# Performance work log

Measured on AMD Instinct MI355X. Metric: run time of the kernel, lower is better.

Reference implementation:

```python
import jax, jax.numpy as jnp
import numpy as np

B, S, D, T, H = 4, 2048, 1024, 5, 8


def setup_inputs() -> dict:
    key = jax.random.key(0)
    ks = jax.random.split(key, 12)
    sc = 0.02  # small init scale for weights so attention logits stay sane
    return {
        "x": jax.random.normal(ks[0], (B, S, D), jnp.float32),
        "time_steps": jax.random.randint(ks[1], (B, S), 0, T),
        "gamma": jnp.ones((T, D), jnp.float32),
        "beta": jax.random.normal(ks[2], (T, D), jnp.float32) * sc,
        "decay": jnp.ones((T,), jnp.float32),
        "shift_W": jax.random.normal(ks[3], (D, D), jnp.float32) * sc,
        "shift_b": jax.random.normal(ks[4], (D,), jnp.float32) * sc,
        "in_proj_W": jax.random.normal(ks[5], (3 * D, D), jnp.float32) * sc,
        "in_proj_b": jax.random.normal(ks[6], (3 * D,), jnp.float32) * sc,
        "out_proj_W": jax.random.normal(ks[7], (D, D), jnp.float32) * sc,
        "out_proj_b": jax.random.normal(ks[8], (D,), jnp.float32) * sc,
    }


def reference(x, time_steps, gamma, beta, decay, shift_W, shift_b,
              in_proj_W, in_proj_b, out_proj_W, out_proj_b):
    eps = 1e-5
    T_ = gamma.shape[0]
    b_, s_, d_ = x.shape
    hd = d_ // H

    # --- per-token indexed LayerNorm + decay (vectorized gather of norm params) ---
    idx = jnp.clip(time_steps, 0, T_ - 1)              # safe gather index [B,S]
    mu = jnp.mean(x, axis=-1, keepdims=True)
    var = jnp.mean(jnp.square(x - mu), axis=-1, keepdims=True)
    xn = (x - mu) * jax.lax.rsqrt(var + eps)           # [B,S,D]
    normed = (xn * gamma[idx] + beta[idx]) * decay[idx][..., None]
    x = jnp.where((time_steps < T_)[..., None], normed, x)

    # --- residual temporal shift (Linear) ---
    x = x + x @ shift_W.T + shift_b

    # --- torch-style MultiheadAttention(x, x, x), batch_first ---
    qkv = x @ in_proj_W.T + in_proj_b                  # [B,S,3D]
    q, k, v = jnp.split(qkv, 3, axis=-1)
    q = q.reshape(b_, s_, H, hd)
    k = k.reshape(b_, s_, H, hd)
    v = v.reshape(b_, s_, H, hd)
    scale = 1.0 / jnp.sqrt(jnp.asarray(hd, x.dtype))
    scores = jnp.einsum('bqhd,bkhd->bhqk', q, k) * scale   # [B,H,S,S]
    attn = jax.nn.softmax(scores, axis=-1)
    ctx = jnp.einsum('bhqk,bkhd->bqhd', attn, v).reshape(b_, s_, d_)
    attended = ctx @ out_proj_W.T + out_proj_b
    return x + attended
```

## Files before the change

kernel.cpp:

```cpp
#include <hip/hip_runtime.h>
#include <math.h>

#define B_ 4
#define S_ 2048
#define D_ 1024
#define T_ 5
#define H_ 8
#define HD_ 128
#define M_ (B_*S_)

typedef __bf16 bf16x8 __attribute__((ext_vector_type(8)));
typedef float  f32x4  __attribute__((ext_vector_type(4)));

__device__ __forceinline__ float bf2f(unsigned short u) {
    union { unsigned int i; float f; } c; c.i = ((unsigned int)u) << 16; return c.f;
}
__device__ __forceinline__ unsigned short f2bf(float f) {
    union { float f; unsigned int i; } c; c.f = f;
    unsigned int u = c.i;
    u += 0x7fffu + ((u >> 16) & 1u);
    return (unsigned short)(u >> 16);
}

__device__ __forceinline__ void gll16(const void* g, void* l) {
    __builtin_amdgcn_global_load_lds(
        (const __attribute__((address_space(1))) void*)g,
        (__attribute__((address_space(3))) void*)l, 16, 0, 0);
}

__global__ __launch_bounds__(256) void f2bf_kernel(
    const float* __restrict__ src, unsigned short* __restrict__ dst)
{
    int i = (blockIdx.x * 256 + threadIdx.x) * 4;
    float4 v = *(const float4*)(src + i);
    ushort4 o;
    o.x = f2bf(v.x); o.y = f2bf(v.y); o.z = f2bf(v.z); o.w = f2bf(v.w);
    *(ushort4*)(dst + i) = o;
}

__global__ __launch_bounds__(256) void ln_kernel(
    const float* __restrict__ x, const int* __restrict__ ts,
    const float* __restrict__ gamma, const float* __restrict__ beta,
    const float* __restrict__ decay, unsigned short* __restrict__ out)
{
    int row = blockIdx.x;
    int tid = threadIdx.x;
    float4 v = ((const float4*)(x + (size_t)row * D_))[tid];
    float s  = v.x + v.y + v.z + v.w;
    float s2 = v.x*v.x + v.y*v.y + v.z*v.z + v.w*v.w;
    #pragma unroll
    for (int off = 32; off; off >>= 1) {
        s  += __shfl_down(s,  off);
        s2 += __shfl_down(s2, off);
    }
    __shared__ float ps[4], ps2[4];
    if ((tid & 63) == 0) { ps[tid >> 6] = s; ps2[tid >> 6] = s2; }
    __syncthreads();
    float tot  = ps[0]  + ps[1]  + ps[2]  + ps[3];
    float tot2 = ps2[0] + ps2[1] + ps2[2] + ps2[3];
    float mu   = tot  * (1.0f / D_);
    float var  = tot2 * (1.0f / D_) - mu * mu;
    float rstd = rsqrtf(var + 1e-5f);

    int t  = ts[row];
    int tc = min(max(t, 0), T_ - 1);
    float4 g = ((const float4*)(gamma + (size_t)tc * D_))[tid];
    float4 b = ((const float4*)(beta  + (size_t)tc * D_))[tid];
    float dec = decay[tc];

    float4 o;
    o.x = ((v.x - mu) * rstd * g.x + b.x) * dec;
    o.y = ((v.y - mu) * rstd * g.y + b.y) * dec;
    o.z = ((v.z - mu) * rstd * g.z + b.z) * dec;
    o.w = ((v.w - mu) * rstd * g.w + b.w) * dec;
    if (t >= T_) o = v;
    ushort4 ob;
    ob.x = f2bf(o.x); ob.y = f2bf(o.y); ob.z = f2bf(o.z); ob.w = f2bf(o.w);
    ((ushort4*)(out + (size_t)row * D_))[tid] = ob;
}

__global__ __launch_bounds__(256) void gemm_mfma(
    const unsigned short* __restrict__ A,
    const unsigned short* __restrict__ Wt,
    const float* __restrict__ bias,
    const float* __restrict__ ResF,
    const unsigned short* __restrict__ ResB,
    float* __restrict__ Cf,
    unsigned short* __restrict__ Cb,
    int M, int N, int K)
{
    __shared__ __align__(16) unsigned short As[128 * 32];
    __shared__ __align__(16) unsigned short Bs[128 * 32];
    int tid  = threadIdx.x;
    int w    = tid >> 6, lane = tid & 63;
    int lm   = lane & 15, quad = lane >> 4;
    int wm   = w & 1,  wn   = w >> 1;
    int i0 = blockIdx.y * 128, j0 = blockIdx.x * 128;

    f32x4 acc[4][4];
    #pragma unroll
    for (int mt = 0; mt < 4; ++mt)
        #pragma unroll
        for (int nt = 0; nt < 4; ++nt)
            acc[mt][nt] = (f32x4){0.f, 0.f, 0.f, 0.f};

    int c0 = w * 128 + lane;
    int r0 = c0 >> 2,   k80 = (c0 & 3) * 8;
    int c1 = c0 + 64;
    int r1 = c1 >> 2,   k81 = (c1 & 3) * 8;

    for (int kt = 0; kt < K; kt += 32) {
        __syncthreads();
        gll16(A  + (size_t)(i0 + r0) * K + kt + k80, As + (size_t)(w * 128 + 0 ) * 8);
        gll16(A  + (size_t)(i0 + r1) * K + kt + k81, As + (size_t)(w * 128 + 64) * 8);
        gll16(Wt + (size_t)(j0 + r0) * K + kt + k80, Bs + (size_t)(w * 128 + 0 ) * 8);
        gll16(Wt + (size_t)(j0 + r1) * K + kt + k81, Bs + (size_t)(w * 128 + 64) * 8);
        __syncthreads();

        bf16x8 af[4], bfr[4];
        #pragma unroll
        for (int mt = 0; mt < 4; ++mt)
            af[mt] = *(const bf16x8*)&As[(wm * 64 + mt * 16 + lm) * 32 + quad * 8];
        #pragma unroll
        for (int nt = 0; nt < 4; ++nt)
            bfr[nt] = *(const bf16x8*)&Bs[(wn * 64 + nt * 16 + lm) * 32 + quad * 8];
        #pragma unroll
        for (int mt = 0; mt < 4; ++mt)
            #pragma unroll
            for (int nt = 0; nt < 4; ++nt)
                acc[mt][nt] = __builtin_amdgcn_mfma_f32_16x16x32_bf16(
                    af[mt], bfr[nt], acc[mt][nt], 0, 0, 0);
    }

    #pragma unroll
    for (int nt = 0; nt < 4; ++nt) {
        int j = j0 + wn * 64 + nt * 16 + lm;
        float bj = bias[j];
        #pragma unroll
        for (int mt = 0; mt < 4; ++mt) {
            #pragma unroll
            for (int r = 0; r < 4; ++r) {
                int i = i0 + wm * 64 + mt * 16 + quad * 4 + r;
                size_t off = (size_t)i * N + j;
                float v = acc[mt][nt][r] + bj;
                if (ResF) v += ResF[off];
                else if (ResB) v += bf2f(ResB[off]);
                if (Cf) Cf[off] = v;
                if (Cb) Cb[off] = f2bf(v);
            }
        }
    }
}

__global__ __launch_bounds__(256) void transpose_v(
    const unsigned short* __restrict__ qkv, unsigned short* __restrict__ vt)
{
    __shared__ unsigned short Ts[64][72];
    int t = threadIdx.x;
    int s0 = blockIdx.x * 64, c0 = blockIdx.y * 64, b = blockIdx.z;
    int r  = t >> 2, cg = (t & 3) * 16;
    const unsigned short* src =
        qkv + (size_t)(b * S_ + s0 + r) * (3 * D_) + 2 * D_ + c0 + cg;
    *(bf16x8*)&Ts[r][cg]     = *(const bf16x8*)(src);
    *(bf16x8*)&Ts[r][cg + 8] = *(const bf16x8*)(src + 8);
    __syncthreads();
    int dd = t >> 2, sg = (t & 3) * 16;
    unsigned short tmp[16];
    #pragma unroll
    for (int j = 0; j < 16; ++j) tmp[j] = Ts[sg + j][dd];
    unsigned short* dst = vt + ((size_t)b * D_ + c0 + dd) * S_ + s0 + sg;
    *(bf16x8*)dst       = *(bf16x8*)&tmp[0];
    *(bf16x8*)(dst + 8) = *(bf16x8*)&tmp[8];
}

__global__ __launch_bounds__(256, 2) void flash_mfma(
    const unsigned short* __restrict__ qkv,
    const unsigned short* __restrict__ vt,
    unsigned short* __restrict__ ctx)
{
    __shared__ unsigned short Ks [64][136];
    __shared__ unsigned short Vts[128][72];
    __shared__ unsigned short Ps [4][32][72];

    int tid  = threadIdx.x;
    int w    = tid >> 6, lane = tid & 63;
    int lm   = lane & 15, quad = lane >> 4;
    int qt = blockIdx.x, h = blockIdx.y, b = blockIdx.z;
    const int rs = 3 * D_;
    const float scale = 0.08838834764831844f;
    size_t qbase  = (size_t)b * S_ * rs + (size_t)h * HD_;
    size_t kbase  = qbase + D_;
    size_t vtbase = ((size_t)b * H_ + h) * (size_t)HD_ * S_;
    int q0 = qt * 128 + w * 32;

    bf16x8 qf[2][4];
    #pragma unroll
    for (int mt = 0; mt < 2; ++mt)
        #pragma unroll
        for (int kc = 0; kc < 4; ++kc) {
            bf16x8 raw = *(const bf16x8*)(
                qkv + qbase + (size_t)(q0 + mt * 16 + lm) * rs + kc * 32 + quad * 8);
            bf16x8 sc;
            #pragma unroll
            for (int j = 0; j < 8; ++j) {
                unsigned short u;
                __builtin_memcpy(&u, (const char*)&raw + 2 * j, 2);
                u = f2bf(bf2f(u) * scale);
                __builtin_memcpy((char*)&sc + 2 * j, &u, 2);
            }
            qf[mt][kc] = sc;
        }

    f32x4 oacc[2][8];
    #pragma unroll
    for (int mt = 0; mt < 2; ++mt)
        #pragma unroll
        for (int n = 0; n < 8; ++n)
            oacc[mt][n] = (f32x4){0.f, 0.f, 0.f, 0.f};
    float lst[2][4];
    #pragma unroll
    for (int mt = 0; mt < 2; ++mt)
        #pragma unroll
        for (int r = 0; r < 4; ++r) lst[mt][r] = 0.f;

    for (int kt = 0; kt < S_ / 64; ++kt) {
        int k0 = kt * 64;
        __syncthreads();
        #pragma unroll
        for (int i = 0; i < 4; ++i) {
            int chunk = tid + 256 * i;
            int r = chunk >> 4, cc = chunk & 15;
            bf16x8 kv8 = *(const bf16x8*)(
                qkv + kbase + (size_t)(k0 + r) * rs + cc * 8);
            *(bf16x8*)&Ks[r][cc * 8] = kv8;
        }
        #pragma unroll
        for (int i = 0; i < 4; ++i) {
            int chunk = tid + 256 * i;
            int d = chunk >> 3, cc = chunk & 7;
            bf16x8 vv8 = *(const bf16x8*)(
                vt + vtbase + (size_t)d * S_ + k0 + cc * 8);
            *(bf16x8*)&Vts[d][cc * 8] = vv8;
        }
        __syncthreads();

        f32x4 sacc[2][4];
        #pragma unroll
        for (int mt = 0; mt < 2; ++mt)
            #pragma unroll
            for (int n = 0; n < 4; ++n)
                sacc[mt][n] = (f32x4){0.f, 0.f, 0.f, 0.f};
        #pragma unroll
        for (int n = 0; n < 4; ++n) {
            bf16x8 bk[4];
            #pragma unroll
            for (int kc = 0; kc < 4; ++kc)
                bk[kc] = *(const bf16x8*)&Ks[n * 16 + lm][kc * 32 + quad * 8];
            #pragma unroll
            for (int mt = 0; mt < 2; ++mt)
                #pragma unroll
                for (int kc = 0; kc < 4; ++kc)
                    sacc[mt][n] = __builtin_amdgcn_mfma_f32_16x16x32_bf16(
                        qf[mt][kc], bk[kc], sacc[mt][n], 0, 0, 0);
        }

        #pragma unroll
        for (int mt = 0; mt < 2; ++mt) {
            #pragma unroll
            for (int r = 0; r < 4; ++r) {
                float p0 = __expf(sacc[mt][0][r]);
                float p1 = __expf(sacc[mt][1][r]);
                float p2 = __expf(sacc[mt][2][r]);
                float p3 = __expf(sacc[mt][3][r]);
                lst[mt][r] += (p0 + p1) + (p2 + p3);
                int row = mt * 16 + quad * 4 + r;
                Ps[w][row][ 0 + lm] = f2bf(p0);
                Ps[w][row][16 + lm] = f2bf(p1);
                Ps[w][row][32 + lm] = f2bf(p2);
                Ps[w][row][48 + lm] = f2bf(p3);
            }
        }

        bf16x8 pa[2][2];
        #pragma unroll
        for (int mt = 0; mt < 2; ++mt)
            #pragma unroll
            for (int kc = 0; kc < 2; ++kc)
                pa[mt][kc] = *(const bf16x8*)&Ps[w][mt * 16 + lm][kc * 32 + quad * 8];
        #pragma unroll
        for (int n = 0; n < 8; ++n) {
            bf16x8 bv0 = *(const bf16x8*)&Vts[n * 16 + lm][quad * 8];
            bf16x8 bv1 = *(const bf16x8*)&Vts[n * 16 + lm][32 + quad * 8];
            #pragma unroll
            for (int mt = 0; mt < 2; ++mt) {
                oacc[mt][n] = __builtin_amdgcn_mfma_f32_16x16x32_bf16(
                    pa[mt][0], bv0, oacc[mt][n], 0, 0, 0);
                oacc[mt][n] = __builtin_amdgcn_mfma_f32_16x16x32_bf16(
                    pa[mt][1], bv1, oacc[mt][n], 0, 0, 0);
            }
        }
    }

    float linv[2][4];
    #pragma unroll
    for (int mt = 0; mt < 2; ++mt)
        #pragma unroll
        for (int r = 0; r < 4; ++r) {
            float l = lst[mt][r];
            l += __shfl_xor(l, 1);
            l += __shfl_xor(l, 2);
            l += __shfl_xor(l, 4);
            l += __shfl_xor(l, 8);
            linv[mt][r] = 1.0f / l;
        }
    size_t rowbase = (size_t)b * S_ + (size_t)qt * 128 + w * 32;
    #pragma unroll
    for (int mt = 0; mt < 2; ++mt)
        #pragma unroll
        for (int r = 0; r < 4; ++r) {
            size_t row = rowbase + mt * 16 + quad * 4 + r;
            unsigned short* dst = ctx + row * D_ + h * HD_ + lm;
            #pragma unroll
            for (int n = 0; n < 8; ++n)
                dst[n * 16] = f2bf(oacc[mt][n][r] * linv[mt][r]);
        }
}

extern "C" void kernel_launch(void* const* d_in, const int* in_sizes, int n_in,
                              void* d_out, int out_size, void* d_ws, size_t ws_size,
                              hipStream_t stream) {
    (void)in_sizes; (void)n_in; (void)out_size; (void)ws_size;
    const float* x          = (const float*)d_in[0];
    const int*   ts         = (const int*)  d_in[1];
    const float* gamma      = (const float*)d_in[2];
    const float* beta       = (const float*)d_in[3];
    const float* decay      = (const float*)d_in[4];
    const float* shift_W    = (const float*)d_in[5];
    const float* shift_b    = (const float*)d_in[6];
    const float* in_proj_W  = (const float*)d_in[7];
    const float* in_proj_b  = (const float*)d_in[8];
    const float* out_proj_W = (const float*)d_in[9];
    const float* out_proj_b = (const float*)d_in[10];
    float* out = (float*)d_out;

    unsigned short* p     = (unsigned short*)d_ws;
    unsigned short* xln_b = p;
    unsigned short* qkv_b = xln_b + (size_t)M_ * D_;
    unsigned short* xs_b  = qkv_b + (size_t)M_ * 3 * D_;
    unsigned short* wsh_b = xs_b  + (size_t)M_ * D_;
    unsigned short* wip_b = wsh_b + (size_t)D_ * D_;
    unsigned short* wop_b = wip_b + (size_t)3 * D_ * D_;
    unsigned short* vt_b  = xs_b;
    unsigned short* ctx_b = xln_b;
    float* xs = out;

    f2bf_kernel<<<D_ * D_ / 1024,     256, 0, stream>>>(shift_W,    wsh_b);
    f2bf_kernel<<<3 * D_ * D_ / 1024, 256, 0, stream>>>(in_proj_W,  wip_b);
    f2bf_kernel<<<D_ * D_ / 1024,     256, 0, stream>>>(out_proj_W, wop_b);

    ln_kernel<<<M_, 256, 0, stream>>>(x, ts, gamma, beta, decay, xln_b);

    gemm_mfma<<<dim3(D_ / 128, M_ / 128), 256, 0, stream>>>(
        xln_b, wsh_b, shift_b, nullptr, xln_b, xs, xs_b, M_, D_, D_);
    gemm_mfma<<<dim3(3 * D_ / 128, M_ / 128), 256, 0, stream>>>(
        xs_b, wip_b, in_proj_b, nullptr, nullptr, nullptr, qkv_b, M_, 3 * D_, D_);

    transpose_v<<<dim3(S_ / 64, D_ / 64, B_), 256, 0, stream>>>(qkv_b, vt_b);
    flash_mfma<<<dim3(S_ / 128, H_, B_), 256, 0, stream>>>(qkv_b, vt_b, ctx_b);

    gemm_mfma<<<dim3(D_ / 128, M_ / 128), 256, 0, stream>>>(
        ctx_b, wop_b, out_proj_b, xs, nullptr, out, nullptr, M_, D_, D_);
}
```

Baseline: 407.3 us.

## Halve flash attention query tile per block and reorder grid for K/V reuse

The flash attention kernel now processes 64 query rows per block (16 per wave) instead of 128, which halves per-thread accumulator and Q-fragment registers and raises the launch-bounds occupancy target from 2 to 3 blocks per CU. The grid becomes 1D with the 32 (batch, head) pairs varying fastest, so concurrently running blocks span many heads, and there are twice as many blocks, which helps fill the GPU. The cost is that each block loads the same K/V tile into LDS for half as much MFMA work, doubling total K/V traffic and the number of block-wide syncs per unit of compute.

```diff
diff --git a/kernel.cpp b/kernel.cpp
--- a/kernel.cpp
+++ b/kernel.cpp
@@ -173,55 +173,50 @@
     *(bf16x8*)(dst + 8) = *(bf16x8*)&tmp[8];
 }
 
-__global__ __launch_bounds__(256, 2) void flash_mfma(
+__global__ __launch_bounds__(256, 3) void flash_mfma(
     const unsigned short* __restrict__ qkv,
     const unsigned short* __restrict__ vt,
     unsigned short* __restrict__ ctx)
 {
     __shared__ unsigned short Ks [64][136];
     __shared__ unsigned short Vts[128][72];
-    __shared__ unsigned short Ps [4][32][72];
+    __shared__ unsigned short Ps [4][16][72];
 
     int tid  = threadIdx.x;
     int w    = tid >> 6, lane = tid & 63;
     int lm   = lane & 15, quad = lane >> 4;
-    int qt = blockIdx.x, h = blockIdx.y, b = blockIdx.z;
+    int blk = blockIdx.x;
+    int bh  = blk & 31;
+    int qt  = blk >> 5;
+    int b   = bh >> 3, h = bh & 7;
     const int rs = 3 * D_;
     const float scale = 0.08838834764831844f;
     size_t qbase  = (size_t)b * S_ * rs + (size_t)h * HD_;
     size_t kbase  = qbase + D_;
     size_t vtbase = ((size_t)b * H_ + h) * (size_t)HD_ * S_;
-    int q0 = qt * 128 + w * 32;
-
-    bf16x8 qf[2][4];
-    #pragma unroll
-    for (int mt = 0; mt < 2; ++mt)
-        #pragma unroll
-        for (int kc = 0; kc < 4; ++kc) {
-            bf16x8 raw = *(const bf16x8*)(
-                qkv + qbase + (size_t)(q0 + mt * 16 + lm) * rs + kc * 32 + quad * 8);
-            bf16x8 sc;
-            #pragma unroll
-            for (int j = 0; j < 8; ++j) {
-                unsigned short u;
-                __builtin_memcpy(&u, (const char*)&raw + 2 * j, 2);
-                u = f2bf(bf2f(u) * scale);
-                __builtin_memcpy((char*)&sc + 2 * j, &u, 2);
-            }
-            qf[mt][kc] = sc;
-        }
-
-    f32x4 oacc[2][8];
-    #pragma unroll
-    for (int mt = 0; mt < 2; ++mt)
-        #pragma unroll
-        for (int n = 0; n < 8; ++n)
-            oacc[mt][n] = (f32x4){0.f, 0.f, 0.f, 0.f};
-    float lst[2][4];
-    #pragma unroll
-    for (int mt = 0; mt < 2; ++mt)
-        #pragma unroll
-        for (int r = 0; r < 4; ++r) lst[mt][r] = 0.f;
+    int q0 = qt * 64 + w * 16;
+
+    bf16x8 qf[4];
+    #pragma unroll
+    for (int kc = 0; kc < 4; ++kc) {
+        bf16x8 raw = *(const bf16x8*)(
+            qkv + qbase + (size_t)(q0 + lm) * rs + kc * 32 + quad * 8);
+        bf16x8 sc;
+        #pragma unroll
+        for (int j = 0; j < 8; ++j) {
+            unsigned short u;
+            __builtin_memcpy(&u, (const char*)&raw + 2 * j, 2);
+            u = f2bf(bf2f(u) * scale);
+            __builtin_memcpy((char*)&sc + 2 * j, &u, 2);
+        }
+        qf[kc] = sc;
+    }
+
+    f32x4 oacc[8];
+    #pragma unroll
+    for (int n = 0; n < 8; ++n)
+        oacc[n] = (f32x4){0.f, 0.f, 0.f, 0.f};
+    float lst[4] = {0.f, 0.f, 0.f, 0.f};
 
     for (int kt = 0; kt < S_ / 64; ++kt) {
         int k0 = kt * 64;
@@ -244,86 +239,68 @@
         }
         __syncthreads();
 
-        f32x4 sacc[2][4];
-        #pragma unroll
-        for (int mt = 0; mt < 2; ++mt)
+        f32x4 sacc[4];
+        #pragma unroll
+        for (int n = 0; n < 4; ++n)
+            sacc[n] = (f32x4){0.f, 0.f, 0.f, 0.f};
+        #pragma unroll
+        for (int n = 0; n < 4; ++n) {
             #pragma unroll
-            for (int n = 0; n < 4; ++n)
-                sacc[mt][n] = (f32x4){0.f, 0.f, 0.f, 0.f};
-        #pragma unroll
-        for (int n = 0; n < 4; ++n) {
-            bf16x8 bk[4];
-            #pragma unroll
-            for (int kc = 0; kc < 4; ++kc)
-                bk[kc] = *(const bf16x8*)&Ks[n * 16 + lm][kc * 32 + quad * 8];
-            #pragma unroll
-            for (int mt = 0; mt < 2; ++mt)
-                #pragma unroll
-                for (int kc = 0; kc < 4; ++kc)
-                    sacc[mt][n] = __builtin_amdgcn_mfma_f32_16x16x32_bf16(
-                        qf[mt][kc], bk[kc], sacc[mt][n], 0, 0, 0);
-        }
-
-        #pragma unroll
-        for (int mt = 0; mt < 2; ++mt) {
-            #pragma unroll
-            for (int r = 0; r < 4; ++r) {
-                float p0 = __expf(sacc[mt][0][r]);
-                float p1 = __expf(sacc[mt][1][r]);
-                float p2 = __expf(sacc[mt][2][r]);
-                float p3 = __expf(sacc[mt][3][r]);
-                lst[mt][r] += (p0 + p1) + (p2 + p3);
-                int row = mt * 16 + quad * 4 + r;
-                Ps[w][row][ 0 + lm] = f2bf(p0);
-                Ps[w][row][16 + lm] = f2bf(p1);
-                Ps[w][row][32 + lm] = f2bf(p2);
-                Ps[w][row][48 + lm] = f2bf(p3);
+            for (int kc = 0; kc < 4; ++kc) {
+                bf16x8 bk = *(const bf16x8*)&Ks[n * 16 + lm][kc * 32 + quad * 8];
+                sacc[n] = __builtin_amdgcn_mfma_f32_16x16x32_bf16(
+                    qf[kc], bk, sacc[n], 0, 0, 0);
             }
         }
 
-        bf16x8 pa[2][2];
-        #pragma unroll
-        for (int mt = 0; mt < 2; ++mt)
-            #pragma unroll
-            for (int kc = 0; kc < 2; ++kc)
-                pa[mt][kc] = *(const bf16x8*)&Ps[w][mt * 16 + lm][kc * 32 + quad * 8];
+        #pragma unroll
+        for (int r = 0; r < 4; ++r) {
+            float p0 = __expf(sacc[0][r]);
+            float p1 = __expf(sacc[1][r]);
+            float p2 = __expf(sacc[2][r]);
+            float p3 = __expf(sacc[3][r]);
+            lst[r] += (p0 + p1) + (p2 + p3);
+            int row = quad * 4 + r;
+            Ps[w][row][ 0 + lm] = f2bf(p0);
+            Ps[w][row][16 + lm] = f2bf(p1);
+            Ps[w][row][32 + lm] = f2bf(p2);
+            Ps[w][row][48 + lm] = f2bf(p3);
+        }
+
+        bf16x8 pa[2];
+        #pragma unroll
+        for (int kc = 0; kc < 2; ++kc)
+            pa[kc] = *(const bf16x8*)&Ps[w][lm][kc * 32 + quad * 8];
         #pragma unroll
         for (int n = 0; n < 8; ++n) {
             bf16x8 bv0 = *(const bf16x8*)&Vts[n * 16 + lm][quad * 8];
             bf16x8 bv1 = *(const bf16x8*)&Vts[n * 16 + lm][32 + quad * 8];
-            #pragma unroll
-            for (int mt = 0; mt < 2; ++mt) {
-                oacc[mt][n] = __builtin_amdgcn_mfma_f32_16x16x32_bf16(
-                    pa[mt][0], bv0, oacc[mt][n], 0, 0, 0);
-                oacc[mt][n] = __builtin_amdgcn_mfma_f32_16x16x32_bf16(
-                    pa[mt][1], bv1, oacc[mt][n], 0, 0, 0);
-            }
-        }
-    }
-
-    float linv[2][4];
-    #pragma unroll
-    for (int mt = 0; mt < 2; ++mt)
-        #pragma unroll
-        for (int r = 0; r < 4; ++r) {
-            float l = lst[mt][r];
-            l += __shfl_xor(l, 1);
-            l += __shfl_xor(l, 2);
-            l += __shfl_xor(l, 4);
-            l += __shfl_xor(l, 8);
-            linv[mt][r] = 1.0f / l;
-        }
-    size_t rowbase = (size_t)b * S_ + (size_t)qt * 128 + w * 32;
-    #pragma unroll
-    for (int mt = 0; mt < 2; ++mt)
-        #pragma unroll
-        for (int r = 0; r < 4; ++r) {
-            size_t row = rowbase + mt * 16 + quad * 4 + r;
-            unsigned short* dst = ctx + row * D_ + h * HD_ + lm;
-            #pragma unroll
-            for (int n = 0; n < 8; ++n)
-                dst[n * 16] = f2bf(oacc[mt][n][r] * linv[mt][r]);
-        }
+            oacc[n] = __builtin_amdgcn_mfma_f32_16x16x32_bf16(
+                pa[0], bv0, oacc[n], 0, 0, 0);
+            oacc[n] = __builtin_amdgcn_mfma_f32_16x16x32_bf16(
+                pa[1], bv1, oacc[n], 0, 0, 0);
+        }
+    }
+
+    float linv[4];
+    #pragma unroll
+    for (int r = 0; r < 4; ++r) {
+        float l = lst[r];
+        l += __shfl_xor(l, 1);
+        l += __shfl_xor(l, 2);
+        l += __shfl_xor(l, 4);
+        l += __shfl_xor(l, 8);
+        linv[r] = 1.0f / l;
+    }
+    size_t rowbase = (size_t)b * S_ + (size_t)qt * 64 + w * 16;
+    #pragma unroll
+    for (int r = 0; r < 4; ++r) {
+        size_t row = rowbase + quad * 4 + r;
+        unsigned short* dst = ctx + row * D_ + h * HD_ + lm;
+        #pragma unroll
+        for (int n = 0; n < 8; ++n)
+            dst[n * 16] = f2bf(oacc[n][r] * linv[r]);
+    }
 }
 
 extern "C" void kernel_launch(void* const* d_in, const int* in_sizes, int n_in,
@@ -366,7 +343,7 @@
         xs_b, wip_b, in_proj_b, nullptr, nullptr, nullptr, qkv_b, M_, 3 * D_, D_);
 
     transpose_v<<<dim3(S_ / 64, D_ / 64, B_), 256, 0, stream>>>(qkv_b, vt_b);
-    flash_mfma<<<dim3(S_ / 128, H_, B_), 256, 0, stream>>>(qkv_b, vt_b, ctx_b);
+    flash_mfma<<<dim3((S_ / 64) * H_ * B_), 256, 0, stream>>>(qkv_b, vt_b, ctx_b);
 
     gemm_mfma<<<dim3(D_ / 128, M_ / 128), 256, 0, stream>>>(
         ctx_b, wop_b, out_proj_b, xs, nullptr, out, nullptr, M_, D_, D_);
```

Result: slower. 442.1 us (+8.5%).
